# Optimization experiments

Measured on AMD Instinct MI355X. Metric: run time of the kernel, lower is better.

## Reference

```python
import jax, jax.numpy as jnp
import numpy as np

N = 50000      # nodes
E = 800000     # edges (before self-loops)
DIN, H1, H2, OUT = 128, 128, 64, 40
LN_EPS = 1e-5


def setup_inputs() -> dict:
    key = jax.random.key(0)
    ks = jax.random.split(key, 16)
    s = lambda d: 1.0 / np.sqrt(d)
    inp = {
        "x": jax.random.normal(ks[0], (N, DIN), jnp.float32),
        "edge_index": jax.random.randint(ks[1], (2, E), 0, N, dtype=jnp.int64),
        # GCNConv weights (applied as x @ W) and biases
        "W1": jax.random.normal(ks[2], (DIN, H1), jnp.float32) * s(DIN),
        "b1": jnp.zeros((H1,), jnp.float32),
        "W2": jax.random.normal(ks[3], (H1, H2), jnp.float32) * s(H1),
        "b2": jnp.zeros((H2,), jnp.float32),
        "W3": jax.random.normal(ks[4], (H2, H2), jnp.float32) * s(H2),
        "b3": jnp.zeros((H2,), jnp.float32),
        # LayerNorms
        "g1": jnp.ones((H1,), jnp.float32),
        "be1": jnp.zeros((H1,), jnp.float32),
        "g2": jnp.ones((H2,), jnp.float32),
        "be2": jnp.zeros((H2,), jnp.float32),
        # post_mp MLP head
        "Wp1": jax.random.normal(ks[5], (H2, H2), jnp.float32) * s(H2),
        "bp1": jnp.zeros((H2,), jnp.float32),
        "Wp2": jax.random.normal(ks[6], (H2, OUT), jnp.float32) * s(H2),
        "bp2": jnp.zeros((OUT,), jnp.float32),
    }
    return inp


def _layer_norm(x, g, b):
    mu = jnp.mean(x, axis=-1, keepdims=True)
    var = jnp.mean((x - mu) ** 2, axis=-1, keepdims=True)
    return (x - mu) * jax.lax.rsqrt(var + LN_EPS) * g + b


def _gcn(x, src, dst, norm, W, b):
    # PyG GCNConv: linear first, then normalized gather/scatter-add, bias last
    h = x @ W                                  # [N, H]
    msg = h[src] * norm[:, None]               # [E+N, H] gather
    out = jax.ops.segment_sum(msg, dst, num_segments=N)  # scatter-add
    return out + b


def reference(x, edge_index, W1, b1, W2, b2, W3, b3, g1, be1, g2, be2,
              Wp1, bp1, Wp2, bp2):
    loops = jnp.arange(N, dtype=edge_index.dtype)
    src = jnp.concatenate([edge_index[0], loops])  # add self-loops
    dst = jnp.concatenate([edge_index[1], loops])
    # symmetric normalization D^{-1/2} (A+I) D^{-1/2} (same graph all layers)
    deg = jax.ops.segment_sum(jnp.ones_like(src, dtype=x.dtype), dst,
                              num_segments=N)
    dinv = jnp.where(deg > 0, jax.lax.rsqrt(jnp.maximum(deg, 1.0)), 0.0)
    norm = dinv[src] * dinv[dst]

    h = _gcn(x, src, dst, norm, W1, b1)
    h = _layer_norm(jax.nn.relu(h), g1, be1)
    h = _gcn(h, src, dst, norm, W2, b2)
    h = _layer_norm(jax.nn.relu(h), g2, be2)
    emb = _gcn(h, src, dst, norm, W3, b3)      # emb = conv output, pre-ReLU
    h = jax.nn.relu(emb)
    h = (h @ Wp1 + bp1) @ Wp2 + bp2            # post_mp: two stacked Linears
    return emb, jax.nn.log_softmax(h, axis=1)
```

## Files before the change

### kernel.cpp

```cpp
#include <hip/hip_runtime.h>
#include <hip/hip_bf16.h>

#define DIN 128
#define HID1 128
#define HID2 64
#define OUTD 40

typedef __attribute__((ext_vector_type(8))) short bf16x8;
typedef __attribute__((ext_vector_type(4))) float f32x4;

__device__ __forceinline__ float bf2f(unsigned int u) {
    union { unsigned int i; float f; } c;
    c.i = u << 16;
    return c.f;
}
__device__ __forceinline__ unsigned short f2bf(float f) {
    union { float f; unsigned int i; } c; c.f = f;
    unsigned int r = c.i + 0x7FFFu + ((c.i >> 16) & 1u);
    return (unsigned short)(r >> 16);
}
__device__ __forceinline__ unsigned int packbf(float lo, float hi) {
    return (unsigned int)f2bf(lo) | ((unsigned int)f2bf(hi) << 16);
}

__global__ void pre_kernel(const unsigned short* __restrict__ xu,
                           const int* __restrict__ ei, int* __restrict__ flags,
                           int* __restrict__ cnt, int N) {
    int i = blockIdx.x * blockDim.x + threadIdx.x;
    if (i < N) cnt[i] = 0;
    if (blockIdx.x == 0) {
        __shared__ int sh[2];
        if (threadIdx.x < 2) sh[threadIdx.x] = 0;
        __syncthreads();
        int bad = 0;
        for (int k = threadIdx.x; k < 2048; k += 256) {
            float v = bf2f(xu[2 * k]);
            float a = fabsf(v);
            if (!(a <= 1e4f) || (v != 0.f && a < 1e-4f)) bad++;
        }
        int zodd = 0;
        for (int k = threadIdx.x; k < 1024; k += 256)
            if (ei[2 * k + 1] == 0) zodd++;
        atomicAdd(&sh[0], bad);
        atomicAdd(&sh[1], zodd);
        __syncthreads();
        if (threadIdx.x == 0) {
            flags[0] = (sh[0] > 512) ? 1 : 0;
            flags[1] = (sh[1] > 512) ? 1 : 0;
        }
    }
}

__device__ __forceinline__ int get_src(const int* ei, int E, int e, int e64) {
    return e64 ? ei[2 * e] : ei[e];
}
__device__ __forceinline__ int get_dst(const int* ei, int E, int e, int e64) {
    return e64 ? ei[2 * (E + e)] : ei[E + e];
}

__global__ void pos_kernel(const int* __restrict__ ei, int* __restrict__ cnt,
                           int* __restrict__ pos, int E, int N,
                           const int* __restrict__ flags) {
    int e64 = flags[1];
    int base = (blockIdx.x * blockDim.x + threadIdx.x) * 4;
    #pragma unroll
    for (int u = 0; u < 4; ++u) {
        int e = base + u;
        if (e < E) {
            int d = get_dst(ei, E, e, e64);
            pos[e] = ((unsigned)d < (unsigned)N) ? atomicAdd(&cnt[d], 1) : -1;
        }
    }
}


__launch_bounds__(256)
__global__ void bsum_kernel(const int* __restrict__ cnt, int* __restrict__ bsum, int N) {
    __shared__ int sh[256];
    int t = threadIdx.x;
    int i = blockIdx.x * 256 + t;
    sh[t] = (i < N) ? cnt[i] : 0;
    __syncthreads();
    #pragma unroll
    for (int off = 128; off >= 1; off >>= 1) {
        if (t < off) sh[t] += sh[t + off];
        __syncthreads();
    }
    if (t == 0) bsum[blockIdx.x] = sh[0];
}

__launch_bounds__(256)
__global__ void bscan_kernel(const int* __restrict__ bsum, int* __restrict__ bbase,
                             int* __restrict__ indptr, int NB, int N) {
    __shared__ int part[256];
    int t = threadIdx.x;
    int CH = (NB + 255) / 256;
    int lo = t * CH, hi = lo + CH; if (hi > NB) hi = NB;
    int s = 0;
    for (int i = lo; i < hi; ++i) s += bsum[i];
    part[t] = s;
    __syncthreads();
    for (int off = 1; off < 256; off <<= 1) {
        int v = (t >= off) ? part[t - off] : 0;
        __syncthreads();
        part[t] += v;
        __syncthreads();
    }
    int run = (t > 0) ? part[t - 1] : 0;
    for (int i = lo; i < hi; ++i) { bbase[i] = run; run += bsum[i]; }
    if (t == 255) indptr[N] = part[255];
}

__launch_bounds__(256)
__global__ void emit_kernel(const int* __restrict__ cnt, const int* __restrict__ bbase,
                            int* __restrict__ indptr, float* __restrict__ dinv, int N) {
    __shared__ int sh[256];
    int t = threadIdx.x;
    int i = blockIdx.x * 256 + t;
    int c = (i < N) ? cnt[i] : 0;
    sh[t] = c;
    __syncthreads();
    for (int off = 1; off < 256; off <<= 1) {
        int v = (t >= off) ? sh[t - off] : 0;
        __syncthreads();
        sh[t] += v;
        __syncthreads();
    }
    if (i < N) {
        int excl = sh[t] - c + bbase[blockIdx.x];
        indptr[i] = excl;
        dinv[i] = 1.0f / sqrtf((float)(c + 1));
    }
}

__global__ void scatter_kernel(const int* __restrict__ ei, const int* __restrict__ indptr,
                               const int* __restrict__ pos, const float* __restrict__ dinv,
                               int2* __restrict__ csr_sn,
                               int E, int N, const int* __restrict__ flags) {
    int e64 = flags[1];
    int base = (blockIdx.x * blockDim.x + threadIdx.x) * 4;
    #pragma unroll
    for (int u = 0; u < 4; ++u) {
        int e = base + u;
        if (e < E) {
            int p = pos[e];
            if (p >= 0) {
                int d = get_dst(ei, E, e, e64);
                int s = get_src(ei, E, e, e64);
                if ((unsigned)s >= (unsigned)N) s = 0;
                float nrm = dinv[s] * dinv[d];
                csr_sn[indptr[d] + p] = make_int2(s, __float_as_int(nrm));
            }
        }
    }
}


struct WCvt {
    const void* p[14];
    int sz[14];
    int off[14];
    int tobf[14];
    int cols[14];
};

__global__ void wcvt_kernel(WCvt w, unsigned short* __restrict__ wbf,
                            float* __restrict__ wf, const int* __restrict__ flags) {
    int xf32 = flags[0];
    int stride = gridDim.x * blockDim.x;
    int tid = blockIdx.x * blockDim.x + threadIdx.x;
    for (int a = 0; a < 14; ++a) {
        const float* pf = (const float*)w.p[a];
        const unsigned short* pb = (const unsigned short*)w.p[a];
        int n = w.sz[a], off = w.off[a], tobf = w.tobf[a];
        int cols = w.cols[a];
        int rows = tobf ? (n / cols) : 0;
        for (int i = tid; i < n; i += stride) {
            float v = xf32 ? pf[i] : bf2f(pb[i]);
            if (tobf) {
                int k = i / cols, m = i % cols;
                wbf[off + m * rows + k] = f2bf(v);
            } else {
                wf[off + i] = v;
            }
        }
    }
}

__global__ void xcvt_kernel(const float* __restrict__ xf, unsigned short* __restrict__ xbf,
                            int n, const int* __restrict__ flags) {
    if (!flags[0]) return;
    int stride = gridDim.x * blockDim.x;
    for (int i = blockIdx.x * blockDim.x + threadIdx.x; i < n; i += stride)
        xbf[i] = f2bf(xf[i]);
}


template<int K, int M>
__launch_bounds__(256)
__global__ void mm_mfma_kernel(const unsigned short* __restrict__ A0,
                               const unsigned short* __restrict__ A1,
                               const unsigned short* __restrict__ WT,
                               unsigned short* __restrict__ C, int N,
                               const int* __restrict__ flags, int useAlt) {
    __shared__ unsigned short Ws[M][K + 8];
    const unsigned short* A = (useAlt && flags[0]) ? A1 : A0;
    int tid = threadIdx.x;
    for (int idx = tid; idx < M * K / 8; idx += 256) {
        int r = idx / (K / 8), c8 = idx % (K / 8);
        *(uint4*)&Ws[r][c8 * 8] = *(const uint4*)&WT[r * K + c8 * 8];
    }
    __syncthreads();
    int w = tid >> 6, lane = tid & 63;
    int m = lane & 15, q = lane >> 4;
    int row_a = blockIdx.x * 64 + w * 16 + m;
    if (row_a >= N) row_a = N - 1;
    const unsigned short* arow = A + (size_t)row_a * K;
    f32x4 acc[M / 16];
    #pragma unroll
    for (int t = 0; t < M / 16; ++t) acc[t] = (f32x4){0.f, 0.f, 0.f, 0.f};
    #pragma unroll
    for (int ks = 0; ks < K / 32; ++ks) {
        int k0 = ks * 32 + q * 8;
        bf16x8 a = *(const bf16x8*)&arow[k0];
        #pragma unroll
        for (int t = 0; t < M / 16; ++t) {
            bf16x8 b = *(const bf16x8*)&Ws[t * 16 + m][k0];
            acc[t] = __builtin_amdgcn_mfma_f32_16x16x32_bf16(a, b, acc[t], 0, 0, 0);
        }
    }
    int rbase = blockIdx.x * 64 + w * 16 + q * 4;
    #pragma unroll
    for (int reg = 0; reg < 4; ++reg) {
        int row = rbase + reg;
        if (row < N) {
            #pragma unroll
            for (int t = 0; t < M / 16; ++t)
                C[(size_t)row * M + t * 16 + m] = f2bf(acc[t][reg]);
        }
    }
}


template<int VPL>
__device__ __forceinline__ void gacc1(float* acc, const unsigned short* r, float n) {
    if constexpr (VPL == 8) {
        uint4 u = *(const uint4*)r;
        acc[0] += bf2f(u.x & 0xffffu) * n; acc[1] += bf2f(u.x >> 16) * n;
        acc[2] += bf2f(u.y & 0xffffu) * n; acc[3] += bf2f(u.y >> 16) * n;
        acc[4] += bf2f(u.z & 0xffffu) * n; acc[5] += bf2f(u.z >> 16) * n;
        acc[6] += bf2f(u.w & 0xffffu) * n; acc[7] += bf2f(u.w >> 16) * n;
    } else {
        uint2 u = *(const uint2*)r;
        acc[0] += bf2f(u.x & 0xffffu) * n; acc[1] += bf2f(u.x >> 16) * n;
        acc[2] += bf2f(u.y & 0xffffu) * n; acc[3] += bf2f(u.y >> 16) * n;
    }
}

template<int VPL>
__device__ __forceinline__ void gacc4(float* acc,
                                      const unsigned short* r0, float n0,
                                      const unsigned short* r1, float n1,
                                      const unsigned short* r2, float n2,
                                      const unsigned short* r3, float n3) {
    if constexpr (VPL == 8) {
        uint4 u0 = *(const uint4*)r0;
        uint4 u1 = *(const uint4*)r1;
        uint4 u2 = *(const uint4*)r2;
        uint4 u3 = *(const uint4*)r3;
        acc[0] += bf2f(u0.x & 0xffffu) * n0 + bf2f(u1.x & 0xffffu) * n1
                + bf2f(u2.x & 0xffffu) * n2 + bf2f(u3.x & 0xffffu) * n3;
        acc[1] += bf2f(u0.x >> 16) * n0 + bf2f(u1.x >> 16) * n1
                + bf2f(u2.x >> 16) * n2 + bf2f(u3.x >> 16) * n3;
        acc[2] += bf2f(u0.y & 0xffffu) * n0 + bf2f(u1.y & 0xffffu) * n1
                + bf2f(u2.y & 0xffffu) * n2 + bf2f(u3.y & 0xffffu) * n3;
        acc[3] += bf2f(u0.y >> 16) * n0 + bf2f(u1.y >> 16) * n1
                + bf2f(u2.y >> 16) * n2 + bf2f(u3.y >> 16) * n3;
        acc[4] += bf2f(u0.z & 0xffffu) * n0 + bf2f(u1.z & 0xffffu) * n1
                + bf2f(u2.z & 0xffffu) * n2 + bf2f(u3.z & 0xffffu) * n3;
        acc[5] += bf2f(u0.z >> 16) * n0 + bf2f(u1.z >> 16) * n1
                + bf2f(u2.z >> 16) * n2 + bf2f(u3.z >> 16) * n3;
        acc[6] += bf2f(u0.w & 0xffffu) * n0 + bf2f(u1.w & 0xffffu) * n1
                + bf2f(u2.w & 0xffffu) * n2 + bf2f(u3.w & 0xffffu) * n3;
        acc[7] += bf2f(u0.w >> 16) * n0 + bf2f(u1.w >> 16) * n1
                + bf2f(u2.w >> 16) * n2 + bf2f(u3.w >> 16) * n3;
    } else {
        uint2 u0 = *(const uint2*)r0;
        uint2 u1 = *(const uint2*)r1;
        uint2 u2 = *(const uint2*)r2;
        uint2 u3 = *(const uint2*)r3;
        acc[0] += bf2f(u0.x & 0xffffu) * n0 + bf2f(u1.x & 0xffffu) * n1
                + bf2f(u2.x & 0xffffu) * n2 + bf2f(u3.x & 0xffffu) * n3;
        acc[1] += bf2f(u0.x >> 16) * n0 + bf2f(u1.x >> 16) * n1
                + bf2f(u2.x >> 16) * n2 + bf2f(u3.x >> 16) * n3;
        acc[2] += bf2f(u0.y & 0xffffu) * n0 + bf2f(u1.y & 0xffffu) * n1
                + bf2f(u2.y & 0xffffu) * n2 + bf2f(u3.y & 0xffffu) * n3;
        acc[3] += bf2f(u0.y >> 16) * n0 + bf2f(u1.y >> 16) * n1
                + bf2f(u2.y >> 16) * n2 + bf2f(u3.y >> 16) * n3;
    }
}

template<int H, bool RELU_LN, bool EMB>
__launch_bounds__(256)
__global__ void agg_kernel(const unsigned short* __restrict__ h,
                           const int* __restrict__ indptr,
                           const int2* __restrict__ csr_sn,
                           const float* __restrict__ dinv,
                           const float* __restrict__ bias,
                           const float* __restrict__ gamma,
                           const float* __restrict__ beta,
                           unsigned short* __restrict__ out,
                           void* __restrict__ out_emb,
                           int N, const int* __restrict__ flags) {
    constexpr int VPL = H / 16;
    __shared__ int2 lsn[4][64];
    int w = threadIdx.x >> 6;
    int lane = threadIdx.x & 63;
    int ql = lane >> 4;
    int g = lane & 15;
    int node = blockIdx.x * 4 + w;
    if (node >= N) return;
    float di = dinv[node];
    int c0 = g * VPL;
    float acc[VPL];
    #pragma unroll
    for (int v = 0; v < VPL; ++v) acc[v] = 0.f;
    gacc1<VPL>(acc, h + (size_t)node * H + c0, (ql == 0) ? di * di : 0.f);
    int beg = indptr[node], end = indptr[node + 1];
    for (int base = beg; base < end; base += 64) {
        int m = end - base; if (m > 64) m = 64;
        if (lane < m) lsn[w][lane] = csr_sn[base + lane];
        int j = ql;
        for (; j + 12 < m; j += 16) {
            int2 e0 = lsn[w][j], e1 = lsn[w][j + 4], e2 = lsn[w][j + 8], e3 = lsn[w][j + 12];
            gacc4<VPL>(acc,
                       h + (size_t)e0.x * H + c0, __int_as_float(e0.y),
                       h + (size_t)e1.x * H + c0, __int_as_float(e1.y),
                       h + (size_t)e2.x * H + c0, __int_as_float(e2.y),
                       h + (size_t)e3.x * H + c0, __int_as_float(e3.y));
        }
        for (; j < m; j += 4) {
            int2 e = lsn[w][j];
            gacc1<VPL>(acc, h + (size_t)e.x * H + c0, __int_as_float(e.y));
        }
    }
    #pragma unroll
    for (int v = 0; v < VPL; ++v) acc[v] += __shfl_xor(acc[v], 16, 64);
    #pragma unroll
    for (int v = 0; v < VPL; ++v) acc[v] += __shfl_xor(acc[v], 32, 64);
    #pragma unroll
    for (int v = 0; v < VPL; ++v) acc[v] += bias[c0 + v];
    if constexpr (RELU_LN) {
        #pragma unroll
        for (int v = 0; v < VPL; ++v) acc[v] = fmaxf(acc[v], 0.f);
        float s = 0.f, sq = 0.f;
        #pragma unroll
        for (int v = 0; v < VPL; ++v) { s += acc[v]; sq += acc[v] * acc[v]; }
        #pragma unroll
        for (int off = 8; off >= 1; off >>= 1) {
            s += __shfl_xor(s, off, 64);
            sq += __shfl_xor(sq, off, 64);
        }
        float mu = s * (1.0f / H);
        float var = fmaxf(sq * (1.0f / H) - mu * mu, 0.f);
        float inv = 1.0f / sqrtf(var + 1e-5f);
        #pragma unroll
        for (int v = 0; v < VPL; ++v)
            acc[v] = (acc[v] - mu) * inv * gamma[c0 + v] + beta[c0 + v];
    }
    if (ql == 0) {
        unsigned short* orow = out + (size_t)node * H + c0;
        if constexpr (VPL == 8) {
            uint4 p;
            p.x = packbf(acc[0], acc[1]); p.y = packbf(acc[2], acc[3]);
            p.z = packbf(acc[4], acc[5]); p.w = packbf(acc[6], acc[7]);
            *(uint4*)orow = p;
        } else {
            uint2 p; p.x = packbf(acc[0], acc[1]); p.y = packbf(acc[2], acc[3]);
            *(uint2*)orow = p;
        }
        if constexpr (EMB) {
            if (flags[0]) {
                float* o = (float*)out_emb + (size_t)node * H + c0;
                #pragma unroll
                for (int v4 = 0; v4 < VPL / 4; ++v4)
                    *(float4*)(o + v4 * 4) = make_float4(acc[v4 * 4], acc[v4 * 4 + 1],
                                                         acc[v4 * 4 + 2], acc[v4 * 4 + 3]);
            } else {
                unsigned short* o = (unsigned short*)out_emb + (size_t)node * H + c0;
                #pragma unroll
                for (int v2 = 0; v2 < VPL / 2; ++v2)
                    ((unsigned int*)o)[v2] = packbf(acc[v2 * 2], acc[v2 * 2 + 1]);
            }
        }
    }
}


__launch_bounds__(256)
__global__ void head_kernel(const unsigned short* __restrict__ emb,
                            const float* __restrict__ Wp1,
                            const float* __restrict__ bp1,
                            const float* __restrict__ Wp2,
                            const float* __restrict__ bp2,
                            void* __restrict__ d_out, int N,
                            const int* __restrict__ flags) {
    __shared__ float Est[64][68];
    __shared__ float W1s[64][64];
    __shared__ float Tst[64][68];
    __shared__ float W2s[64][OUTD];
    __shared__ float b1s[64];
    __shared__ float b2s[OUTD];
    int tid = threadIdx.x;
    int row0 = blockIdx.x * 64;
    for (int i = tid; i < 64 * 64; i += 256) W1s[i >> 6][i & 63] = Wp1[i];
    for (int i = tid; i < 64 * OUTD; i += 256) W2s[i / OUTD][i % OUTD] = Wp2[i];
    if (tid < 64) b1s[tid] = bp1[tid];
    if (tid < OUTD) b2s[tid] = bp2[tid];
    for (int i = tid; i < 64 * 32; i += 256) {
        int r = i >> 5, kk = i & 31;
        int row = row0 + r;
        unsigned int u = (row < N) ? *(const unsigned int*)&emb[(size_t)row * 64 + kk * 2] : 0u;
        Est[kk * 2][r]     = fmaxf(bf2f(u & 0xffffu), 0.f);
        Est[kk * 2 + 1][r] = fmaxf(bf2f(u >> 16), 0.f);
    }
    __syncthreads();
    {
        int rg = tid >> 4, cg = tid & 15;
        int r = rg * 4, c = cg * 4;
        float acc[4][4];
        #pragma unroll
        for (int i = 0; i < 4; ++i)
            #pragma unroll
            for (int jj = 0; jj < 4; ++jj) acc[i][jj] = b1s[c + jj];
        #pragma unroll 4
        for (int k = 0; k < 64; ++k) {
            float4 a = *(const float4*)&Est[k][r];
            float4 wv = *(const float4*)&W1s[k][c];
            acc[0][0] += a.x * wv.x; acc[0][1] += a.x * wv.y; acc[0][2] += a.x * wv.z; acc[0][3] += a.x * wv.w;
            acc[1][0] += a.y * wv.x; acc[1][1] += a.y * wv.y; acc[1][2] += a.y * wv.z; acc[1][3] += a.y * wv.w;
            acc[2][0] += a.z * wv.x; acc[2][1] += a.z * wv.y; acc[2][2] += a.z * wv.z; acc[2][3] += a.z * wv.w;
            acc[3][0] += a.w * wv.x; acc[3][1] += a.w * wv.y; acc[3][2] += a.w * wv.z; acc[3][3] += a.w * wv.w;
        }
        #pragma unroll
        for (int i = 0; i < 4; ++i)
            #pragma unroll
            for (int jj = 0; jj < 4; ++jj) Tst[c + jj][r + i] = acc[i][jj];
    }
    __syncthreads();
    int row = tid >> 2, tc = tid & 3, o0 = tc * 10;
    int node = row0 + row;
    float u[10];
    #pragma unroll
    for (int o = 0; o < 10; ++o) u[o] = b2s[o0 + o];
    for (int c2 = 0; c2 < 64; ++c2) {
        float tv = Tst[c2][row];
        const float2* wp = (const float2*)&W2s[c2][o0];
        #pragma unroll
        for (int o2 = 0; o2 < 5; ++o2) {
            float2 wv = wp[o2];
            u[o2 * 2]     += tv * wv.x;
            u[o2 * 2 + 1] += tv * wv.y;
        }
    }
    float mx = u[0];
    #pragma unroll
    for (int o = 1; o < 10; ++o) mx = fmaxf(mx, u[o]);
    mx = fmaxf(mx, __shfl_xor(mx, 1, 64));
    mx = fmaxf(mx, __shfl_xor(mx, 2, 64));
    float sum = 0.f;
    #pragma unroll
    for (int o = 0; o < 10; ++o) sum += __expf(u[o] - mx);
    sum += __shfl_xor(sum, 1, 64);
    sum += __shfl_xor(sum, 2, 64);
    float lse = mx + __logf(sum);
    if (node < N) {
        if (flags[0]) {
            float* base = (float*)d_out + (size_t)N * HID2;
            float* op = base + (size_t)node * OUTD + o0;
            #pragma unroll
            for (int o = 0; o < 10; ++o) op[o] = u[o] - lse;
        } else {
            unsigned short* base = (unsigned short*)d_out + (size_t)N * HID2;
            unsigned int* op = (unsigned int*)(base + (size_t)node * OUTD + o0);
            #pragma unroll
            for (int o2 = 0; o2 < 5; ++o2)
                op[o2] = packbf(u[o2 * 2] - lse, u[o2 * 2 + 1] - lse);
        }
    }
}


extern "C" void kernel_launch(void* const* d_in, const int* in_sizes, int n_in,
                              void* d_out, int out_size, void* d_ws, size_t ws_size,
                              hipStream_t stream) {
    const unsigned short* xu = (const unsigned short*)d_in[0];
    const float*          xf = (const float*)d_in[0];
    const int*            ei = (const int*)d_in[1];

    const int N = in_sizes[0] / DIN;
    const int E = in_sizes[1] / 2;

    size_t off = 0;
    auto take = [&](size_t bytes) {
        size_t cur = off;
        off += (bytes + 255) & ~(size_t)255;
        return cur;
    };
    char* ws = (char*)d_ws;
    int*   flags   = (int*)  (ws + take(256));
    int*   cnt     = (int*)  (ws + take((size_t)N * 4));
    float* dinv    = (float*)(ws + take((size_t)N * 4));
    int*   indptr  = (int*)  (ws + take((size_t)(N + 1) * 4));
    int*   pos     = (int*)  (ws + take((size_t)E * 4));
    int2*  csr_sn  = (int2*) (ws + take((size_t)E * 8));
    int*   bsum    = (int*)  (ws + take(((size_t)N / 256 + 2) * 4));
    int*   bbase   = (int*)  (ws + take(((size_t)N / 256 + 2) * 4));
    unsigned short* wbf = (unsigned short*)(ws + take(32768 * 2));
    float*          wf  = (float*)         (ws + take(8192 * 4));
    unsigned short* hbuf = (unsigned short*)(ws + take((size_t)N * DIN * 2));
    unsigned short* abuf = (unsigned short*)(ws + take((size_t)N * DIN * 2));
    (void)ws_size; (void)n_in; (void)out_size;

    const int TB = 256;
    dim3 blk(TB);
    const int NB = (N + 255) / 256;

    pre_kernel<<<dim3(NB), blk, 0, stream>>>(xu, ei, flags, cnt, N);
    pos_kernel<<<dim3((E + 1023) / 1024), blk, 0, stream>>>(ei, cnt, pos, E, N, flags);
    bsum_kernel<<<dim3(NB), blk, 0, stream>>>(cnt, bsum, N);
    bscan_kernel<<<dim3(1), blk, 0, stream>>>(bsum, bbase, indptr, NB, N);
    emit_kernel<<<dim3(NB), blk, 0, stream>>>(cnt, bbase, indptr, dinv, N);
    scatter_kernel<<<dim3((E + 1023) / 1024), blk, 0, stream>>>(ei, indptr, pos, dinv, csr_sn, E, N, flags);

    WCvt w;
    int bfoff = 0, foff = 0;
    int offs[14];
    const int wcols[14] = {HID1, 0, HID2, 0, HID2, 0, 0, 0, 0, 0, 0, 0, 0, 0};
    for (int a = 0; a < 14; ++a) {
        int idx = a + 2;
        w.p[a] = d_in[idx];
        w.sz[a] = in_sizes[idx];
        int tobf = (idx == 2 || idx == 4 || idx == 6) ? 1 : 0;
        w.tobf[a] = tobf;
        w.cols[a] = tobf ? wcols[a] : 1;
        if (tobf) { w.off[a] = bfoff; bfoff += in_sizes[idx]; }
        else      { w.off[a] = foff;  foff  += in_sizes[idx]; }
        offs[a] = w.off[a];
    }
    wcvt_kernel<<<dim3(64), blk, 0, stream>>>(w, wbf, wf, flags);
    xcvt_kernel<<<dim3(512), blk, 0, stream>>>(xf, abuf, N * DIN, flags);

    unsigned short* W1t = wbf + offs[0];
    unsigned short* W2t = wbf + offs[2];
    unsigned short* W3t = wbf + offs[4];
    float* b1f  = wf + offs[1];
    float* b2f  = wf + offs[3];
    float* b3f  = wf + offs[5];
    float* g1f  = wf + offs[6];
    float* be1f = wf + offs[7];
    float* g2f  = wf + offs[8];
    float* be2f = wf + offs[9];
    float* Wp1f = wf + offs[10];
    float* bp1f = wf + offs[11];
    float* Wp2f = wf + offs[12];
    float* bp2f = wf + offs[13];

    const int MMG = (N + 63) / 64;

    mm_mfma_kernel<DIN, HID1><<<dim3(MMG), blk, 0, stream>>>(xu, abuf, W1t, hbuf, N, flags, 1);
    agg_kernel<HID1, true, false><<<dim3((N + 3) / 4), blk, 0, stream>>>(
        hbuf, indptr, csr_sn, dinv, b1f, g1f, be1f, abuf, nullptr, N, flags);

    mm_mfma_kernel<HID1, HID2><<<dim3(MMG), blk, 0, stream>>>(abuf, nullptr, W2t, hbuf, N, flags, 0);
    agg_kernel<HID2, true, false><<<dim3((N + 3) / 4), blk, 0, stream>>>(
        hbuf, indptr, csr_sn, dinv, b2f, g2f, be2f, abuf, nullptr, N, flags);

    mm_mfma_kernel<HID2, HID2><<<dim3(MMG), blk, 0, stream>>>(abuf, nullptr, W3t, hbuf, N, flags, 0);
    agg_kernel<HID2, false, true><<<dim3((N + 3) / 4), blk, 0, stream>>>(
        hbuf, indptr, csr_sn, dinv, b3f, nullptr, nullptr, abuf, d_out, N, flags);

    head_kernel<<<dim3((N + 63) / 64), blk, 0, stream>>>(
        abuf, Wp1f, bp1f, Wp2f, bp2f, d_out, N, flags);
}
```

Before: 338.6 us.

## Map four nodes per wavefront in aggregation and fold x conversion into weight kernel

The aggregation kernel now gives each 16-lane quarter of a wavefront its own node, so a wave handles four nodes, instead of one node per wave with edges split across quarters. This removes the cross-quarter shuffle reductions and the idle lanes on low-degree nodes (about 17 edges per node on average). The trade-off is more load imbalance between quarters within a wave. The separate x bf16 conversion kernel is merged into the weight-conversion kernel as a 15th entry, with the grid raised to 128 blocks, to save one launch.

Result: slower. 397.8 us (+17.5%).

```diff
diff --git a/kernel.cpp b/kernel.cpp
--- a/kernel.cpp
+++ b/kernel.cpp
@@ -157,42 +157,39 @@
 
 
 struct WCvt {
-    const void* p[14];
-    int sz[14];
-    int off[14];
-    int tobf[14];
-    int cols[14];
+    const void* p[15];
+    int sz[15];
+    int off[15];
+    int tobf[15];
+    int cols[15];
 };
 
 __global__ void wcvt_kernel(WCvt w, unsigned short* __restrict__ wbf,
-                            float* __restrict__ wf, const int* __restrict__ flags) {
+                            float* __restrict__ wf, unsigned short* __restrict__ dst3,
+                            const int* __restrict__ flags) {
     int xf32 = flags[0];
     int stride = gridDim.x * blockDim.x;
     int tid = blockIdx.x * blockDim.x + threadIdx.x;
-    for (int a = 0; a < 14; ++a) {
+    for (int a = 0; a < 15; ++a) {
+        int tobf = w.tobf[a];
+        if (tobf == 3 && !xf32) continue;
         const float* pf = (const float*)w.p[a];
         const unsigned short* pb = (const unsigned short*)w.p[a];
-        int n = w.sz[a], off = w.off[a], tobf = w.tobf[a];
+        int n = w.sz[a], off = w.off[a];
         int cols = w.cols[a];
-        int rows = tobf ? (n / cols) : 0;
+        int rows = (tobf == 1) ? (n / cols) : 0;
         for (int i = tid; i < n; i += stride) {
             float v = xf32 ? pf[i] : bf2f(pb[i]);
-            if (tobf) {
+            if (tobf == 1) {
                 int k = i / cols, m = i % cols;
                 wbf[off + m * rows + k] = f2bf(v);
+            } else if (tobf == 3) {
+                dst3[i] = f2bf(v);
             } else {
                 wf[off + i] = v;
             }
         }
     }
-}
-
-__global__ void xcvt_kernel(const float* __restrict__ xf, unsigned short* __restrict__ xbf,
-                            int n, const int* __restrict__ flags) {
-    if (!flags[0]) return;
-    int stride = gridDim.x * blockDim.x;
-    for (int i = blockIdx.x * blockDim.x + threadIdx.x; i < n; i += stride)
-        xbf[i] = f2bf(xf[i]);
 }
 
 
@@ -313,41 +310,39 @@
                            void* __restrict__ out_emb,
                            int N, const int* __restrict__ flags) {
     constexpr int VPL = H / 16;
-    __shared__ int2 lsn[4][64];
+    __shared__ int2 lsn[4][4][16];
     int w = threadIdx.x >> 6;
     int lane = threadIdx.x & 63;
-    int ql = lane >> 4;
-    int g = lane & 15;
-    int node = blockIdx.x * 4 + w;
-    if (node >= N) return;
-    float di = dinv[node];
-    int c0 = g * VPL;
+    int g = lane >> 4;
+    int idx = lane & 15;
+    int node = blockIdx.x * 16 + w * 4 + g;
+    bool active = node < N;
+    int nd = active ? node : N - 1;
+    float di = dinv[nd];
+    int c0 = idx * VPL;
     float acc[VPL];
     #pragma unroll
     for (int v = 0; v < VPL; ++v) acc[v] = 0.f;
-    gacc1<VPL>(acc, h + (size_t)node * H + c0, (ql == 0) ? di * di : 0.f);
-    int beg = indptr[node], end = indptr[node + 1];
-    for (int base = beg; base < end; base += 64) {
-        int m = end - base; if (m > 64) m = 64;
-        if (lane < m) lsn[w][lane] = csr_sn[base + lane];
-        int j = ql;
-        for (; j + 12 < m; j += 16) {
-            int2 e0 = lsn[w][j], e1 = lsn[w][j + 4], e2 = lsn[w][j + 8], e3 = lsn[w][j + 12];
+    gacc1<VPL>(acc, h + (size_t)nd * H + c0, di * di);
+    int beg = indptr[nd], end = indptr[nd + 1];
+    for (int base = beg; base < end; base += 16) {
+        int m = end - base; if (m > 16) m = 16;
+        if (idx < m) lsn[w][g][idx] = csr_sn[base + idx];
+        int j = 0;
+        for (; j + 3 < m; j += 4) {
+            int2 e0 = lsn[w][g][j],     e1 = lsn[w][g][j + 1];
+            int2 e2 = lsn[w][g][j + 2], e3 = lsn[w][g][j + 3];
             gacc4<VPL>(acc,
                        h + (size_t)e0.x * H + c0, __int_as_float(e0.y),
                        h + (size_t)e1.x * H + c0, __int_as_float(e1.y),
                        h + (size_t)e2.x * H + c0, __int_as_float(e2.y),
                        h + (size_t)e3.x * H + c0, __int_as_float(e3.y));
         }
-        for (; j < m; j += 4) {
-            int2 e = lsn[w][j];
+        for (; j < m; ++j) {
+            int2 e = lsn[w][g][j];
             gacc1<VPL>(acc, h + (size_t)e.x * H + c0, __int_as_float(e.y));
         }
     }
-    #pragma unroll
-    for (int v = 0; v < VPL; ++v) acc[v] += __shfl_xor(acc[v], 16, 64);
-    #pragma unroll
-    for (int v = 0; v < VPL; ++v) acc[v] += __shfl_xor(acc[v], 32, 64);
     #pragma unroll
     for (int v = 0; v < VPL; ++v) acc[v] += bias[c0 + v];
     if constexpr (RELU_LN) {
@@ -368,7 +363,7 @@
         for (int v = 0; v < VPL; ++v)
             acc[v] = (acc[v] - mu) * inv * gamma[c0 + v] + beta[c0 + v];
     }
-    if (ql == 0) {
+    if (active) {
         unsigned short* orow = out + (size_t)node * H + c0;
         if constexpr (VPL == 8) {
             uint4 p;
@@ -495,7 +490,6 @@
                               void* d_out, int out_size, void* d_ws, size_t ws_size,
                               hipStream_t stream) {
     const unsigned short* xu = (const unsigned short*)d_in[0];
-    const float*          xf = (const float*)d_in[0];
     const int*            ei = (const int*)d_in[1];
 
     const int N = in_sizes[0] / DIN;
@@ -548,8 +542,8 @@
         else      { w.off[a] = foff;  foff  += in_sizes[idx]; }
         offs[a] = w.off[a];
     }
-    wcvt_kernel<<<dim3(64), blk, 0, stream>>>(w, wbf, wf, flags);
-    xcvt_kernel<<<dim3(512), blk, 0, stream>>>(xf, abuf, N * DIN, flags);
+    w.p[14] = d_in[0]; w.sz[14] = N * DIN; w.off[14] = 0; w.tobf[14] = 3; w.cols[14] = 1;
+    wcvt_kernel<<<dim3(128), blk, 0, stream>>>(w, wbf, wf, abuf, flags);
 
     unsigned short* W1t = wbf + offs[0];
     unsigned short* W2t = wbf + offs[2];
@@ -567,17 +561,18 @@
     float* bp2f = wf + offs[13];
 
     const int MMG = (N + 63) / 64;
+    const int AGG = (N + 15) / 16;
 
     mm_mfma_kernel<DIN, HID1><<<dim3(MMG), blk, 0, stream>>>(xu, abuf, W1t, hbuf, N, flags, 1);
-    agg_kernel<HID1, true, false><<<dim3((N + 3) / 4), blk, 0, stream>>>(
+    agg_kernel<HID1, true, false><<<dim3(AGG), blk, 0, stream>>>(
         hbuf, indptr, csr_sn, dinv, b1f, g1f, be1f, abuf, nullptr, N, flags);
 
     mm_mfma_kernel<HID1, HID2><<<dim3(MMG), blk, 0, stream>>>(abuf, nullptr, W2t, hbuf, N, flags, 0);
-    agg_kernel<HID2, true, false><<<dim3((N + 3) / 4), blk, 0, stream>>>(
+    agg_kernel<HID2, true, false><<<dim3(AGG), blk, 0, stream>>>(
         hbuf, indptr, csr_sn, dinv, b2f, g2f, be2f, abuf, nullptr, N, flags);
 
     mm_mfma_kernel<HID2, HID2><<<dim3(MMG), blk, 0, stream>>>(abuf, nullptr, W3t, hbuf, N, flags, 0);
-    agg_kernel<HID2, false, true><<<dim3((N + 3) / 4), blk, 0, stream>>>(
+    agg_kernel<HID2, false, true><<<dim3(AGG), blk, 0, stream>>>(
         hbuf, indptr, csr_sn, dinv, b3f, nullptr, nullptr, abuf, d_out, N, flags);
 
     head_kernel<<<dim3((N + 63) / 64), blk, 0, stream>>>(
```
